# Kernel tuning notes

Measured on AMD Instinct MI355X. Metric: run time of the kernel, lower is better.

## Reference

```python
import jax, jax.numpy as jnp
import numpy as np

N, E, IN, OUT, H = 20000, 640000, 256, 64, 4


def setup_inputs() -> dict:
    key = jax.random.key(0)
    ks = jax.random.split(key, 10)
    x = jax.random.normal(ks[0], (N, IN), dtype=jnp.float32)
    edge_index = jax.random.randint(ks[1], (2, E), 0, N, dtype=jnp.int64)
    s1 = 1.0 / np.sqrt(IN)
    s2 = 1.0 / np.sqrt(H * OUT)
    return {
        "x": x,
        "edge_index": edge_index,
        "W1": jax.random.normal(ks[2], (IN, H * OUT), dtype=jnp.float32) * s1,
        "att_src1": jax.random.normal(ks[3], (H, OUT), dtype=jnp.float32) * s2,
        "att_dst1": jax.random.normal(ks[4], (H, OUT), dtype=jnp.float32) * s2,
        "bias1": jnp.zeros((H * OUT,), dtype=jnp.float32),
        "W2": jax.random.normal(ks[5], (H * OUT, OUT), dtype=jnp.float32) * s2,
        "att_src2": jax.random.normal(ks[6], (1, OUT), dtype=jnp.float32) * (1.0 / np.sqrt(OUT)),
        "att_dst2": jax.random.normal(ks[7], (1, OUT), dtype=jnp.float32) * (1.0 / np.sqrt(OUT)),
        "bias2": jnp.zeros((OUT,), dtype=jnp.float32),
    }


def _gat_layer(x, src, dst, W, att_src, att_dst, bias, concat):
    n = x.shape[0]
    h_, c = att_src.shape
    h = (x @ W).reshape(n, h_, c)                     # [N,H,C]
    a_src = jnp.einsum("nhc,hc->nh", h, att_src)      # [N,H]
    a_dst = jnp.einsum("nhc,hc->nh", h, att_dst)
    e = jax.nn.leaky_relu(a_src[src] + a_dst[dst], 0.2)  # [E,H]
    m = jax.ops.segment_max(e, dst, num_segments=n)
    e = jnp.exp(e - m[dst])
    denom = jax.ops.segment_sum(e, dst, num_segments=n)
    alpha = e / (denom[dst] + 1e-16)                  # edge softmax over dst groups
    out = jax.ops.segment_sum(alpha[:, :, None] * h[src], dst, num_segments=n)  # [N,H,C]
    out = out.reshape(n, h_ * c) if concat else out.mean(axis=1)
    return out + bias


def reference(x, edge_index, W1, att_src1, att_dst1, bias1, W2, att_src2, att_dst2, bias2):
    n = x.shape[0]
    loops = jnp.arange(n, dtype=edge_index.dtype)
    ei = jnp.concatenate([edge_index, jnp.stack([loops, loops])], axis=1)  # add self-loops
    src, dst = ei[0], ei[1]
    # eval mode: dropout layers are identity
    x1 = jax.nn.elu(_gat_layer(x, src, dst, W1, att_src1, att_dst1, bias1, concat=True))
    x2 = _gat_layer(x1, src, dst, W2, att_src2, att_dst2, bias2, concat=False)
    return x2
```

## Files before the change

kernel.cpp:

```cpp
#include <hip/hip_runtime.h>
#include <hip/hip_bf16.h>
#include <math.h>

#define NN   20000
#define INF  256
#define HID  256
#define NH   4
#define OUTF 64

__device__ __forceinline__ float lrelu(float x){ return x > 0.f ? x : 0.2f*x; }
__device__ __forceinline__ float elu(float x){ return x > 0.f ? x : __expf(x)-1.f; }

__global__ void k_deg_init(int* deg){
    int i = blockIdx.x*blockDim.x + threadIdx.x;
    if (i < NN) deg[i] = 1;
}

__global__ void k_deg_hist(const int* __restrict__ ei, int* deg, int E){
    int e = blockIdx.x*blockDim.x + threadIdx.x;
    if (e < E) atomicAdd(&deg[ei[E + e]], 1);
}

__global__ void k_scan(const int* __restrict__ deg, int* __restrict__ rowptr){
    __shared__ int part[1024];
    int t = threadIdx.x;
    const int CH = 20;
    int base = t*CH;
    int s = 0;
    for (int i = 0; i < CH; i++){ int idx = base+i; if (idx < NN) s += deg[idx]; }
    part[t] = s;
    __syncthreads();
    for (int off = 1; off < 1024; off <<= 1){
        int v = (t >= off) ? part[t-off] : 0;
        __syncthreads();
        part[t] += v;
        __syncthreads();
    }
    int run = (t > 0) ? part[t-1] : 0;
    for (int i = 0; i < CH; i++){
        int idx = base+i;
        if (idx < NN){ rowptr[idx] = run; run += deg[idx]; }
    }
    if (t == 1023) rowptr[NN] = part[1023];
}

__global__ void k_selfloop(const int* __restrict__ rowptr, int* col, int* cursor){
    int n = blockIdx.x*blockDim.x + threadIdx.x;
    if (n < NN){ int p = rowptr[n]; col[p] = n; cursor[n] = p+1; }
}

__global__ void k_scatter(const int* __restrict__ ei, int* cursor, int* col, int E){
    int e = blockIdx.x*blockDim.x + threadIdx.x;
    if (e < E){
        int s = ei[e], d = ei[E + e];
        int pos = atomicAdd(&cursor[d], 1);
        col[pos] = s;
    }
}

__global__ void k_gemm1(const float* __restrict__ x, const float* __restrict__ W,
                        const float* __restrict__ att_s, const float* __restrict__ att_d,
                        __hip_bfloat16* __restrict__ h1b, float* __restrict__ as1,
                        float* __restrict__ ad1){
    __shared__ float xs[16][INF];
    int row0 = blockIdx.x*16;
    int t = threadIdx.x;
    int lane = t & 63, wv = t >> 6;
    for (int i = t; i < 16*INF; i += 256)
        xs[i>>8][i&255] = x[(size_t)(row0 + (i>>8))*INF + (i&255)];
    __syncthreads();
    float acc[16];
    #pragma unroll
    for (int r = 0; r < 16; r++) acc[r] = 0.f;
    for (int k = 0; k < INF; k++){
        float w = W[k*HID + t];
        #pragma unroll
        for (int r = 0; r < 16; r++) acc[r] = fmaf(xs[r][k], w, acc[r]);
    }
    float sv = att_s[t], dv = att_d[t];
    #pragma unroll
    for (int r = 0; r < 16; r++){
        h1b[(size_t)(row0+r)*HID + t] = __float2bfloat16(acc[r]);
        float ps = acc[r]*sv, pd = acc[r]*dv;
        #pragma unroll
        for (int off = 32; off >= 1; off >>= 1){
            ps += __shfl_xor(ps, off, 64);
            pd += __shfl_xor(pd, off, 64);
        }
        if (lane == 0){
            as1[(row0+r)*NH + wv] = ps;
            ad1[(row0+r)*NH + wv] = pd;
        }
    }
}

__global__ void k_agg1(const ushort* __restrict__ h1b, const int* __restrict__ rowptr,
                       const int* __restrict__ col, const float* __restrict__ as1,
                       const float* __restrict__ ad1, const float* __restrict__ bias,
                       float* __restrict__ x1){
    int wv = threadIdx.x >> 6, lane = threadIdx.x & 63;
    int n = blockIdx.x*4 + wv;
    if (n >= NN) return;
    int beg = rowptr[n], end = rowptr[n+1];
    float4 adst = ((const float4*)ad1)[n];
    int h = lane >> 4;
    float adh = h==0?adst.x : h==1?adst.y : h==2?adst.z : adst.w;
    float den = 0.f;
    float4 accs[4];
    #pragma unroll
    for (int u = 0; u < 4; u++) accs[u] = make_float4(0.f,0.f,0.f,0.f);

    for (int base = beg; base < end; base += 64){
        int cnt = min(64, end - base);
        int myidx = (lane < cnt) ? col[base + lane] : 0;
        int j = 0;
        for (; j + 8 <= cnt; j += 8){
            int ss[8];
            #pragma unroll
            for (int u = 0; u < 8; u++) ss[u] = __shfl(myidx, j+u, 64);
            uint2 hv[8];
            float aw[8];
            #pragma unroll
            for (int u = 0; u < 8; u++){
                hv[u] = *(const uint2*)(h1b + ((size_t)ss[u]<<8) + (lane<<2));
                aw[u] = as1[ss[u]*NH + h];
            }
            #pragma unroll
            for (int u = 0; u < 8; u++){
                float w = __expf(lrelu(aw[u]+adh));
                den += w;
                float f0 = __uint_as_float(hv[u].x << 16);
                float f1 = __uint_as_float(hv[u].x & 0xFFFF0000u);
                float f2 = __uint_as_float(hv[u].y << 16);
                float f3 = __uint_as_float(hv[u].y & 0xFFFF0000u);
                accs[u&3].x = fmaf(w, f0, accs[u&3].x);
                accs[u&3].y = fmaf(w, f1, accs[u&3].y);
                accs[u&3].z = fmaf(w, f2, accs[u&3].z);
                accs[u&3].w = fmaf(w, f3, accs[u&3].w);
            }
        }
        for (; j < cnt; j++){
            int s0 = __shfl(myidx, j, 64);
            uint2 hv0 = *(const uint2*)(h1b + ((size_t)s0<<8) + (lane<<2));
            float aw0 = as1[s0*NH + h];
            float w = __expf(lrelu(aw0+adh));
            den += w;
            accs[0].x = fmaf(w, __uint_as_float(hv0.x << 16),        accs[0].x);
            accs[0].y = fmaf(w, __uint_as_float(hv0.x & 0xFFFF0000u), accs[0].y);
            accs[0].z = fmaf(w, __uint_as_float(hv0.y << 16),        accs[0].z);
            accs[0].w = fmaf(w, __uint_as_float(hv0.y & 0xFFFF0000u), accs[0].w);
        }
    }
    float rs = 1.f/(den + 1e-16f);
    float4 b = ((const float4*)bias)[lane];
    float4 o;
    o.x = elu((accs[0].x+accs[1].x+accs[2].x+accs[3].x)*rs + b.x);
    o.y = elu((accs[0].y+accs[1].y+accs[2].y+accs[3].y)*rs + b.y);
    o.z = elu((accs[0].z+accs[1].z+accs[2].z+accs[3].z)*rs + b.z);
    o.w = elu((accs[0].w+accs[1].w+accs[2].w+accs[3].w)*rs + b.w);
    ((float4*)(x1 + (size_t)n*HID))[lane] = o;
}

__global__ void k_gemm2(const float* __restrict__ x1, const float* __restrict__ W2,
                        const float* __restrict__ att_s, const float* __restrict__ att_d,
                        float* __restrict__ h2, float* __restrict__ a2s,
                        float* __restrict__ a2d){
    __shared__ float xs[32][HID];
    int row0 = blockIdx.x*32;
    int t = threadIdx.x;
    for (int i = t; i < 32*HID; i += 256)
        xs[i>>8][i&255] = x1[(size_t)(row0 + (i>>8))*HID + (i&255)];
    __syncthreads();
    int c  = t & 63;
    int r0 = (t >> 6)*8;
    float acc[8];
    #pragma unroll
    for (int r = 0; r < 8; r++) acc[r] = 0.f;
    for (int k = 0; k < HID; k++){
        float w = W2[k*OUTF + c];
        #pragma unroll
        for (int r = 0; r < 8; r++) acc[r] = fmaf(xs[r0+r][k], w, acc[r]);
    }
    float sv = att_s[c], dv = att_d[c];
    #pragma unroll
    for (int r = 0; r < 8; r++){
        h2[(size_t)(row0+r0+r)*OUTF + c] = acc[r];
        float ps = acc[r]*sv, pd = acc[r]*dv;
        #pragma unroll
        for (int off = 32; off >= 1; off >>= 1){
            ps += __shfl_xor(ps, off, 64);
            pd += __shfl_xor(pd, off, 64);
        }
        if (c == 0){
            a2s[row0+r0+r] = ps;
            a2d[row0+r0+r] = pd;
        }
    }
}

__global__ void k_agg2(const float* __restrict__ h2, const int* __restrict__ rowptr,
                       const int* __restrict__ col, const float* __restrict__ a2s,
                       const float* __restrict__ a2d, const float* __restrict__ bias2,
                       float* __restrict__ out){
    int wv = threadIdx.x >> 6, lane = threadIdx.x & 63;
    int n = blockIdx.x*4 + wv;
    if (n >= NN) return;
    int beg = rowptr[n], end = rowptr[n+1];
    float adh = a2d[n];
    float den = 0.f;
    float acc[4] = {0.f, 0.f, 0.f, 0.f};
    for (int base = beg; base < end; base += 64){
        int cnt = min(64, end - base);
        int myidx = (lane < cnt) ? col[base + lane] : 0;
        int j = 0;
        for (; j + 8 <= cnt; j += 8){
            int ss[8];
            #pragma unroll
            for (int u = 0; u < 8; u++) ss[u] = __shfl(myidx, j+u, 64);
            float hw[8], aw[8];
            #pragma unroll
            for (int u = 0; u < 8; u++){
                hw[u] = h2[(size_t)ss[u]*OUTF + lane];
                aw[u] = a2s[ss[u]];
            }
            #pragma unroll
            for (int u = 0; u < 8; u++){
                float w = __expf(lrelu(aw[u]+adh));
                den += w;
                acc[u&3] = fmaf(w, hw[u], acc[u&3]);
            }
        }
        for (; j < cnt; j++){
            int s0 = __shfl(myidx, j, 64);
            float hv0 = h2[(size_t)s0*OUTF + lane];
            float w0 = __expf(lrelu(a2s[s0]+adh));
            den += w0;
            acc[0] = fmaf(w0, hv0, acc[0]);
        }
    }
    out[(size_t)n*OUTF + lane] = (acc[0]+acc[1]+acc[2]+acc[3])/(den + 1e-16f) + bias2[lane];
}

extern "C" void kernel_launch(void* const* d_in, const int* in_sizes, int n_in,
                              void* d_out, int out_size, void* d_ws, size_t ws_size,
                              hipStream_t stream){
    const float* x      = (const float*)d_in[0];
    const int*   ei     = (const int*)  d_in[1];
    const float* W1     = (const float*)d_in[2];
    const float* att_s1 = (const float*)d_in[3];
    const float* att_d1 = (const float*)d_in[4];
    const float* bias1  = (const float*)d_in[5];
    const float* W2     = (const float*)d_in[6];
    const float* att_s2 = (const float*)d_in[7];
    const float* att_d2 = (const float*)d_in[8];
    const float* bias2  = (const float*)d_in[9];
    int E = in_sizes[1] / 2;

    char* w = (char*)d_ws;
    size_t off = 0;
    auto alloc = [&](size_t b){ void* p = w + off; off += (b + 255) & ~(size_t)255; return p; };
    __hip_bfloat16* h1b = (__hip_bfloat16*)alloc((size_t)NN*HID*2);
    float* x1     = (float*)alloc((size_t)NN*HID*4);
    float* h2     = (float*)alloc((size_t)NN*OUTF*4);
    float* as1    = (float*)alloc((size_t)NN*NH*4);
    float* ad1    = (float*)alloc((size_t)NN*NH*4);
    float* a2s    = (float*)alloc((size_t)NN*4);
    float* a2d    = (float*)alloc((size_t)NN*4);
    int*   deg    = (int*)alloc((size_t)(NN+1)*4);
    int*   rowptr = (int*)alloc((size_t)(NN+1)*4);
    int*   cursor = (int*)alloc((size_t)NN*4);
    int*   col    = (int*)alloc((size_t)(E+NN)*4);

    k_deg_init<<<(NN+255)/256, 256, 0, stream>>>(deg);
    k_deg_hist<<<(E+255)/256, 256, 0, stream>>>(ei, deg, E);
    k_scan<<<1, 1024, 0, stream>>>(deg, rowptr);
    k_selfloop<<<(NN+255)/256, 256, 0, stream>>>(rowptr, col, cursor);
    k_scatter<<<(E+255)/256, 256, 0, stream>>>(ei, cursor, col, E);

    k_gemm1<<<NN/16, 256, 0, stream>>>(x, W1, att_s1, att_d1, h1b, as1, ad1);
    k_agg1<<<(NN+3)/4, 256, 0, stream>>>((const ushort*)h1b, rowptr, col, as1, ad1, bias1, x1);

    k_gemm2<<<NN/32, 256, 0, stream>>>(x1, W2, att_s2, att_d2, h2, a2s, a2d);
    k_agg2<<<(NN+3)/4, 256, 0, stream>>>(h2, rowptr, col, a2s, a2d, bias2, (float*)d_out);
}
```

Before: 324.8 us.

## Register-block both GEMMs with 4-column float4 tiles and 64-row blocks

Both dense projection kernels are restructured so each thread computes a 4-column by multi-row register tile. They read W as float4 and x rows from shared memory as float4, and load the input tile with vectorized, bounds-clamped loads. This raises arithmetic intensity and cuts global and LDS load instructions per FMA. The attention reductions shrink to 16-lane shuffles and the bf16 stores become 4-wide. The larger tiles increase register and LDS pressure (64 KB shared per block), which may reduce occupancy.

```diff
diff --git a/kernel.cpp b/kernel.cpp
--- a/kernel.cpp
+++ b/kernel.cpp
@@ -10,6 +10,18 @@
 
 __device__ __forceinline__ float lrelu(float x){ return x > 0.f ? x : 0.2f*x; }
 __device__ __forceinline__ float elu(float x){ return x > 0.f ? x : __expf(x)-1.f; }
+__device__ __forceinline__ ushort f2bf(float f){
+    unsigned u = __float_as_uint(f);
+    u += 0x7FFF + ((u >> 16) & 1);
+    return (ushort)(u >> 16);
+}
+__device__ __forceinline__ void fma4(float4& a, float s, const float4& b){
+    a.x = fmaf(s, b.x, a.x); a.y = fmaf(s, b.y, a.y);
+    a.z = fmaf(s, b.z, a.z); a.w = fmaf(s, b.w, a.w);
+}
+__device__ __forceinline__ float dot4(float4 a, float4 b){
+    return a.x*b.x + a.y*b.y + a.z*b.z + a.w*b.w;
+}
 
 __global__ void k_deg_init(int* deg){
     int i = blockIdx.x*blockDim.x + threadIdx.x;
@@ -60,36 +72,57 @@
 
 __global__ void k_gemm1(const float* __restrict__ x, const float* __restrict__ W,
                         const float* __restrict__ att_s, const float* __restrict__ att_d,
-                        __hip_bfloat16* __restrict__ h1b, float* __restrict__ as1,
+                        ushort* __restrict__ h1b, float* __restrict__ as1,
                         float* __restrict__ ad1){
-    __shared__ float xs[16][INF];
-    int row0 = blockIdx.x*16;
+    __shared__ float xs[64][INF];
+    int row0 = blockIdx.x*64;
     int t = threadIdx.x;
-    int lane = t & 63, wv = t >> 6;
-    for (int i = t; i < 16*INF; i += 256)
-        xs[i>>8][i&255] = x[(size_t)(row0 + (i>>8))*INF + (i&255)];
+    for (int i = t; i < 64*(INF/4); i += 256){
+        int r = i >> 6, kq = i & 63;
+        int gr = row0 + r; if (gr >= NN) gr = NN-1;
+        ((float4*)&xs[r][0])[kq] = ((const float4*)(x + (size_t)gr*INF))[kq];
+    }
     __syncthreads();
-    float acc[16];
-    #pragma unroll
-    for (int r = 0; r < 16; r++) acc[r] = 0.f;
-    for (int k = 0; k < INF; k++){
-        float w = W[k*HID + t];
+    int cg = t & 63;
+    int rg = t >> 6;
+    const float* Wc = W + 4*cg;
+    float4 acc[16];
+    #pragma unroll
+    for (int r = 0; r < 16; r++) acc[r] = make_float4(0.f,0.f,0.f,0.f);
+    for (int k4 = 0; k4 < INF; k4 += 4){
+        float4 w0 = *(const float4*)(Wc + (size_t)(k4+0)*HID);
+        float4 w1 = *(const float4*)(Wc + (size_t)(k4+1)*HID);
+        float4 w2 = *(const float4*)(Wc + (size_t)(k4+2)*HID);
+        float4 w3 = *(const float4*)(Wc + (size_t)(k4+3)*HID);
         #pragma unroll
-        for (int r = 0; r < 16; r++) acc[r] = fmaf(xs[r][k], w, acc[r]);
-    }
-    float sv = att_s[t], dv = att_d[t];
+        for (int r = 0; r < 16; r++){
+            float4 xv = *(const float4*)(&xs[rg*16+r][k4]);
+            fma4(acc[r], xv.x, w0); fma4(acc[r], xv.y, w1);
+            fma4(acc[r], xv.z, w2); fma4(acc[r], xv.w, w3);
+        }
+    }
+    float4 sv = *(const float4*)(att_s + 4*cg);
+    float4 dv = *(const float4*)(att_d + 4*cg);
+    int hh = cg >> 4;
     #pragma unroll
     for (int r = 0; r < 16; r++){
-        h1b[(size_t)(row0+r)*HID + t] = __float2bfloat16(acc[r]);
-        float ps = acc[r]*sv, pd = acc[r]*dv;
+        int row = row0 + rg*16 + r;
+        float ps = dot4(acc[r], sv);
+        float pd = dot4(acc[r], dv);
         #pragma unroll
-        for (int off = 32; off >= 1; off >>= 1){
+        for (int off = 1; off < 16; off <<= 1){
             ps += __shfl_xor(ps, off, 64);
             pd += __shfl_xor(pd, off, 64);
         }
-        if (lane == 0){
-            as1[(row0+r)*NH + wv] = ps;
-            ad1[(row0+r)*NH + wv] = pd;
+        if (row < NN){
+            ushort4 hb;
+            hb.x = f2bf(acc[r].x); hb.y = f2bf(acc[r].y);
+            hb.z = f2bf(acc[r].z); hb.w = f2bf(acc[r].w);
+            *(ushort4*)(h1b + (size_t)row*HID + 4*cg) = hb;
+            if ((cg & 15) == 0){
+                as1[row*NH + hh] = ps;
+                ad1[row*NH + hh] = pd;
+            }
         }
     }
 }
@@ -127,28 +160,28 @@
             }
             #pragma unroll
             for (int u = 0; u < 8; u++){
-                float w = __expf(lrelu(aw[u]+adh));
-                den += w;
+                float wexp = __expf(lrelu(aw[u]+adh));
+                den += wexp;
                 float f0 = __uint_as_float(hv[u].x << 16);
                 float f1 = __uint_as_float(hv[u].x & 0xFFFF0000u);
                 float f2 = __uint_as_float(hv[u].y << 16);
                 float f3 = __uint_as_float(hv[u].y & 0xFFFF0000u);
-                accs[u&3].x = fmaf(w, f0, accs[u&3].x);
-                accs[u&3].y = fmaf(w, f1, accs[u&3].y);
-                accs[u&3].z = fmaf(w, f2, accs[u&3].z);
-                accs[u&3].w = fmaf(w, f3, accs[u&3].w);
+                accs[u&3].x = fmaf(wexp, f0, accs[u&3].x);
+                accs[u&3].y = fmaf(wexp, f1, accs[u&3].y);
+                accs[u&3].z = fmaf(wexp, f2, accs[u&3].z);
+                accs[u&3].w = fmaf(wexp, f3, accs[u&3].w);
             }
         }
         for (; j < cnt; j++){
             int s0 = __shfl(myidx, j, 64);
             uint2 hv0 = *(const uint2*)(h1b + ((size_t)s0<<8) + (lane<<2));
             float aw0 = as1[s0*NH + h];
-            float w = __expf(lrelu(aw0+adh));
-            den += w;
-            accs[0].x = fmaf(w, __uint_as_float(hv0.x << 16),        accs[0].x);
-            accs[0].y = fmaf(w, __uint_as_float(hv0.x & 0xFFFF0000u), accs[0].y);
-            accs[0].z = fmaf(w, __uint_as_float(hv0.y << 16),        accs[0].z);
-            accs[0].w = fmaf(w, __uint_as_float(hv0.y & 0xFFFF0000u), accs[0].w);
+            float wexp = __expf(lrelu(aw0+adh));
+            den += wexp;
+            accs[0].x = fmaf(wexp, __uint_as_float(hv0.x << 16),         accs[0].x);
+            accs[0].y = fmaf(wexp, __uint_as_float(hv0.x & 0xFFFF0000u), accs[0].y);
+            accs[0].z = fmaf(wexp, __uint_as_float(hv0.y << 16),         accs[0].z);
+            accs[0].w = fmaf(wexp, __uint_as_float(hv0.y & 0xFFFF0000u), accs[0].w);
         }
     }
     float rs = 1.f/(den + 1e-16f);
@@ -165,35 +198,51 @@
                         const float* __restrict__ att_s, const float* __restrict__ att_d,
                         float* __restrict__ h2, float* __restrict__ a2s,
                         float* __restrict__ a2d){
-    __shared__ float xs[32][HID];
-    int row0 = blockIdx.x*32;
+    __shared__ float xs[64][HID];
+    int row0 = blockIdx.x*64;
     int t = threadIdx.x;
-    for (int i = t; i < 32*HID; i += 256)
-        xs[i>>8][i&255] = x1[(size_t)(row0 + (i>>8))*HID + (i&255)];
+    for (int i = t; i < 64*(HID/4); i += 256){
+        int r = i >> 6, kq = i & 63;
+        int gr = row0 + r; if (gr >= NN) gr = NN-1;
+        ((float4*)&xs[r][0])[kq] = ((const float4*)(x1 + (size_t)gr*HID))[kq];
+    }
     __syncthreads();
-    int c  = t & 63;
-    int r0 = (t >> 6)*8;
-    float acc[8];
-    #pragma unroll
-    for (int r = 0; r < 8; r++) acc[r] = 0.f;
-    for (int k = 0; k < HID; k++){
-        float w = W2[k*OUTF + c];
+    int cg = t & 15;
+    int rg = t >> 4;
+    const float* Wc = W2 + 4*cg;
+    float4 acc[4];
+    #pragma unroll
+    for (int r = 0; r < 4; r++) acc[r] = make_float4(0.f,0.f,0.f,0.f);
+    for (int k4 = 0; k4 < HID; k4 += 4){
+        float4 w0 = *(const float4*)(Wc + (size_t)(k4+0)*OUTF);
+        float4 w1 = *(const float4*)(Wc + (size_t)(k4+1)*OUTF);
+        float4 w2 = *(const float4*)(Wc + (size_t)(k4+2)*OUTF);
+        float4 w3 = *(const float4*)(Wc + (size_t)(k4+3)*OUTF);
         #pragma unroll
-        for (int r = 0; r < 8; r++) acc[r] = fmaf(xs[r0+r][k], w, acc[r]);
-    }
-    float sv = att_s[c], dv = att_d[c];
-    #pragma unroll
-    for (int r = 0; r < 8; r++){
-        h2[(size_t)(row0+r0+r)*OUTF + c] = acc[r];
-        float ps = acc[r]*sv, pd = acc[r]*dv;
+        for (int r = 0; r < 4; r++){
+            float4 xv = *(const float4*)(&xs[rg*4+r][k4]);
+            fma4(acc[r], xv.x, w0); fma4(acc[r], xv.y, w1);
+            fma4(acc[r], xv.z, w2); fma4(acc[r], xv.w, w3);
+        }
+    }
+    float4 sv = *(const float4*)(att_s + 4*cg);
+    float4 dv = *(const float4*)(att_d + 4*cg);
+    #pragma unroll
+    for (int r = 0; r < 4; r++){
+        int row = row0 + rg*4 + r;
+        float ps = dot4(acc[r], sv);
+        float pd = dot4(acc[r], dv);
         #pragma unroll
-        for (int off = 32; off >= 1; off >>= 1){
+        for (int off = 1; off < 16; off <<= 1){
             ps += __shfl_xor(ps, off, 64);
             pd += __shfl_xor(pd, off, 64);
         }
-        if (c == 0){
-            a2s[row0+r0+r] = ps;
-            a2d[row0+r0+r] = pd;
+        if (row < NN){
+            *(float4*)(h2 + (size_t)row*OUTF + 4*cg) = acc[r];
+            if (cg == 0){
+                a2s[row] = ps;
+                a2d[row] = pd;
+            }
         }
     }
 }
@@ -225,9 +274,9 @@
             }
             #pragma unroll
             for (int u = 0; u < 8; u++){
-                float w = __expf(lrelu(aw[u]+adh));
-                den += w;
-                acc[u&3] = fmaf(w, hw[u], acc[u&3]);
+                float wexp = __expf(lrelu(aw[u]+adh));
+                den += wexp;
+                acc[u&3] = fmaf(wexp, hw[u], acc[u&3]);
             }
         }
         for (; j < cnt; j++){
@@ -259,7 +308,7 @@
     char* w = (char*)d_ws;
     size_t off = 0;
     auto alloc = [&](size_t b){ void* p = w + off; off += (b + 255) & ~(size_t)255; return p; };
-    __hip_bfloat16* h1b = (__hip_bfloat16*)alloc((size_t)NN*HID*2);
+    ushort* h1b   = (ushort*)alloc((size_t)NN*HID*2);
     float* x1     = (float*)alloc((size_t)NN*HID*4);
     float* h2     = (float*)alloc((size_t)NN*OUTF*4);
     float* as1    = (float*)alloc((size_t)NN*NH*4);
@@ -277,9 +326,9 @@
     k_selfloop<<<(NN+255)/256, 256, 0, stream>>>(rowptr, col, cursor);
     k_scatter<<<(E+255)/256, 256, 0, stream>>>(ei, cursor, col, E);
 
-    k_gemm1<<<NN/16, 256, 0, stream>>>(x, W1, att_s1, att_d1, h1b, as1, ad1);
-    k_agg1<<<(NN+3)/4, 256, 0, stream>>>((const ushort*)h1b, rowptr, col, as1, ad1, bias1, x1);
-
-    k_gemm2<<<NN/32, 256, 0, stream>>>(x1, W2, att_s2, att_d2, h2, a2s, a2d);
+    k_gemm1<<<(NN+63)/64, 256, 0, stream>>>(x, W1, att_s1, att_d1, h1b, as1, ad1);
+    k_agg1<<<(NN+3)/4, 256, 0, stream>>>(h1b, rowptr, col, as1, ad1, bias1, x1);
+
+    k_gemm2<<<(NN+63)/64, 256, 0, stream>>>(x1, W2, att_s2, att_d2, h2, a2s, a2d);
     k_agg2<<<(NN+3)/4, 256, 0, stream>>>(h2, rowptr, col, a2s, a2d, bias2, (float*)d_out);
 }
```

Result: slower. 472.2 us (+45.4%).
